# Kernel optimization log

Measured on AMD Instinct MI355X. Metric: run time of the kernel, lower is better.

## Reference

```python
import jax, jax.numpy as jnp
import numpy as np

INPUT_SIZE = 200
HIDDEN_SIZE = 100
B, T = 64, 2048


def setup_inputs() -> dict:
    key = jax.random.key(0)
    k_x, k_wi, k_wh, k_bi, k_bh = jax.random.split(key, 5)
    s = 1.0 / np.sqrt(HIDDEN_SIZE)  # PyTorch LSTM init range
    x = jax.random.normal(k_x, (B, T, INPUT_SIZE), dtype=jnp.float32)
    W_ih = jax.random.uniform(k_wi, (4 * HIDDEN_SIZE, INPUT_SIZE), minval=-s, maxval=s, dtype=jnp.float32)
    W_hh = jax.random.uniform(k_wh, (4 * HIDDEN_SIZE, HIDDEN_SIZE), minval=-s, maxval=s, dtype=jnp.float32)
    b_ih = jax.random.uniform(k_bi, (4 * HIDDEN_SIZE,), minval=-s, maxval=s, dtype=jnp.float32)
    b_hh = jax.random.uniform(k_bh, (4 * HIDDEN_SIZE,), minval=-s, maxval=s, dtype=jnp.float32)
    return {"x": x, "W_ih": W_ih, "W_hh": W_hh, "b_ih": b_ih, "b_hh": b_hh}


def reference(x, W_ih, W_hh, b_ih, b_hh):
    # Single-layer batch_first LSTM; returns output[:, -1] == final hidden state h_T.
    Bb, Tt, _ = x.shape
    H = W_hh.shape[1]
    # Precompute input projections for all timesteps: [T, B, 4H]
    xg = jnp.einsum('bti,gi->tbg', x, W_ih) + (b_ih + b_hh)

    def step(carry, xt):
        h, c = carry
        gates = xt + h @ W_hh.T  # [B, 4H]
        i, f, g, o = jnp.split(gates, 4, axis=-1)  # PyTorch gate order: i,f,g,o
        i = jax.nn.sigmoid(i)
        f = jax.nn.sigmoid(f)
        g = jnp.tanh(g)
        o = jax.nn.sigmoid(o)
        c = f * c + i * g
        h = o * jnp.tanh(c)
        return (h, c), None

    h0 = jnp.zeros((Bb, H), dtype=x.dtype)
    c0 = jnp.zeros((Bb, H), dtype=x.dtype)
    (hT, _), _ = jax.lax.scan(step, (h0, c0), xg)
    return hT  # [B, H]
```

## Files before the change

### kernel.cpp

```cpp
#include <hip/hip_runtime.h>
#include <math.h>


#define T_TOTAL 2048
#define B_SZ 64
#define IN_SZ 200
#define H_SZ 100
#define GP 512
#define KP 112
#define NPROD 192
#define NBLK 256

typedef float v2f __attribute__((ext_vector_type(2)));

__device__ __forceinline__ float sigf(float x) {
    return __builtin_amdgcn_rcpf(1.f + __expf(-x));
}

#define QSWAP(x, ctrl) \
    __int_as_float(__builtin_amdgcn_mov_dpp(__float_as_int(x), ctrl, 0xF, 0xF, true))
#define QBCAST(x, ctrl) QSWAP(x, ctrl)

#define LDS_BARRIER()                                          \
    do {                                                       \
        asm volatile("s_waitcnt lgkmcnt(0)" ::: "memory");     \
        __builtin_amdgcn_s_barrier();                          \
    } while (0)

__global__ void prep_kernel(const float* __restrict__ W_ih,
                            const float* __restrict__ W_hh,
                            const float* __restrict__ b_ih,
                            const float* __restrict__ b_hh,
                            float* __restrict__ Wt,
                            float* __restrict__ bias,
                            float* __restrict__ Whp,
                            unsigned int* __restrict__ sync) {
    int idx = blockIdx.x * 256 + threadIdx.x;
    if (idx < IN_SZ * GP) {
        int k = idx >> 9;
        int g = idx & (GP - 1);
        Wt[idx] = (g < 400) ? W_ih[g * IN_SZ + k] : 0.f;
    }
    if (idx < GP) bias[idx] = (idx < 400) ? (b_ih[idx] + b_hh[idx]) : 0.f;
    if (idx < 400 * KP) {
        int g = idx / KP;
        int k = idx - g * KP;
        Whp[idx] = (k < H_SZ) ? W_hh[g * H_SZ + k] : 0.f;
    }
    if (idx < 64) sync[idx] = 0u;
}

__global__ __attribute__((amdgpu_flat_work_group_size(512, 512), amdgpu_waves_per_eu(2, 2)))
void fused_kernel(const float* __restrict__ x,
                  const float* __restrict__ Wt,
                  const float* __restrict__ bias,
                  const float* __restrict__ Whp,
                  float* __restrict__ xg,
                  float* __restrict__ out,
                  unsigned int* __restrict__ sync,
                  int TC, int NB, int nch) {
    __shared__ __align__(16) float hlds[2][KP];
    __shared__ __align__(16) float xTc[2][50][68];
    __shared__ __align__(16) float4 LW[50][32];

    const int bid = blockIdx.x;
    const int tid = threadIdx.x;
    unsigned int* done = sync;
    unsigned int* freed = sync + 32;
    const size_t slot_sz = (size_t)B_SZ * TC * GP;

    if (bid < B_SZ) {
        const int b = bid;
        const int q = tid >> 2;
        const int s4 = tid & 3;
        const bool active = (q < H_SZ);
        const int qc = active ? q : (H_SZ - 1);
        const bool o1 = (s4 & 1) != 0;
        const bool o2 = (s4 & 2) != 0;
        const float asc  = (s4 == 2) ? 2.f : 1.f;
        const float amul = (s4 == 2) ? 2.f : 1.f;
        const float aadd = (s4 == 2) ? -1.f : 0.f;

        v2f w[4][14];
        if (active) {
            const v2f* W2 = (const v2f*)Whp;
#pragma unroll
            for (int g = 0; g < 4; ++g) {
                const v2f* row = W2 + (size_t)(g * H_SZ + q) * (KP / 2) + s4 * 14;
#pragma unroll
                for (int m = 0; m < 14; ++m) w[g][m] = row[m];
            }
        } else {
#pragma unroll
            for (int g = 0; g < 4; ++g)
#pragma unroll
                for (int m = 0; m < 14; ++m) { w[g][m].x = 0.f; w[g][m].y = 0.f; }
        }

        float c = 0.f;
        if (tid < KP) hlds[0][tid] = 0.f;
        if (tid < KP - H_SZ) hlds[1][H_SZ + tid] = 0.f;
        __syncthreads();

        const size_t lane_off = (size_t)(s4 * H_SZ + qc);
        float hval = 0.f;

#define LSTM_STEP(XB, RB, WB, KOFF)                                            \
    {                                                                          \
        const float4* hb4 = (const float4*)&hlds[RB][s4 * 28];                 \
        float4 h4 = hb4[0];                                                    \
        v2f hlo; hlo.x = h4.x; hlo.y = h4.y;                                   \
        v2f hhi; hhi.x = h4.z; hhi.y = h4.w;                                   \
        v2f a0[4], a1[4];                                                      \
        _Pragma("unroll") for (int g = 0; g < 4; ++g) {                        \
            a0[g] = hlo * w[g][0];                                             \
            a1[g] = hhi * w[g][1];                                             \
        }                                                                      \
        _Pragma("unroll") for (int m = 1; m < 7; ++m) {                        \
            h4 = hb4[m];                                                       \
            hlo.x = h4.x; hlo.y = h4.y;                                        \
            hhi.x = h4.z; hhi.y = h4.w;                                        \
            _Pragma("unroll") for (int g = 0; g < 4; ++g) {                    \
                a0[g] = __builtin_elementwise_fma(hlo, w[g][2 * m], a0[g]);    \
                a1[g] = __builtin_elementwise_fma(hhi, w[g][2 * m + 1], a1[g]);\
            }                                                                  \
        }                                                                      \
        float p[4];                                                            \
        _Pragma("unroll") for (int g = 0; g < 4; ++g) {                        \
            v2f sv = a0[g] + a1[g];                                            \
            p[g] = sv.x + sv.y;                                                \
        }                                                                      \
        float e01 = o1 ? p[0] : p[1];                                          \
        float r01 = (o1 ? p[1] : p[0]) + QSWAP(e01, 0xB1);                     \
        float e23 = o1 ? p[2] : p[3];                                          \
        float r23 = (o1 ? p[3] : p[2]) + QSWAP(e23, 0xB1);                     \
        float ecx = o2 ? r01 : r23;                                            \
        float dwn = (o2 ? r23 : r01) + QSWAP(ecx, 0x4E) + XB;                  \
        XB = xq[(KOFF) * GP];                                                  \
        float act = __builtin_fmaf(sigf(asc * dwn), amul, aadd);               \
        float vi = QBCAST(act, 0x00);                                          \
        float vf = QBCAST(act, 0x55);                                          \
        float vg = QBCAST(act, 0xAA);                                          \
        float vo = QBCAST(act, 0xFF);                                          \
        c = __builtin_fmaf(vf, c, vi * vg);                                    \
        float tcv = __builtin_fmaf(sigf(2.f * c), 2.f, -1.f);                  \
        hval = vo * tcv;                                                       \
        if (active && s4 == 0) hlds[WB][q] = hval;                             \
        LDS_BARRIER();                                                         \
    }

        for (int k = 0; k < nch; ++k) {
            if (tid == 0) {
                while (atomicAdd(&done[k], 0u) < (unsigned)NPROD)
                    __builtin_amdgcn_s_sleep(8);
                __threadfence();
            }
            __syncthreads();

            const float* xp = xg + (size_t)(k % NB) * slot_sz + (size_t)b * TC * GP + lane_off;
            float xr0 = xp[0 * GP];
            float xr1 = xp[1 * GP];
            float xr2 = xp[2 * GP];
            float xr3 = xp[3 * GP];
            const float* xq = xp + 4 * GP;

            for (int tl = 0; tl < TC; tl += 4) {
                LSTM_STEP(xr0, 0, 1, 0);
                LSTM_STEP(xr1, 1, 0, 1);
                LSTM_STEP(xr2, 0, 1, 2);
                LSTM_STEP(xr3, 1, 0, 3);
                xq += 4 * GP;
            }
            if (tid == 0) atomicAdd(&freed[k], 1u);
        }
#undef LSTM_STEP

        if (active && s4 == 0) out[b * H_SZ + q] = hval;

    } else {
        const int pid = bid - B_SZ;
        const int h = tid >> 8;
        const int t2 = tid & 255;
        const int gt = t2 & 15;
        const int tt = t2 >> 4;
        const int TPB = TC >> 7;
        const int njobs = B_SZ * TPB * 4;
        const float2* x2 = (const float2*)x;
        const float4* Wt4 = (const float4*)Wt;
        const float4* bias4 = (const float4*)bias;

        for (int k = 0; k < nch; ++k) {
            if (k >= NB) {
                if (tid == 0)
                    while (atomicAdd(&freed[k - NB], 0u) < (unsigned)B_SZ)
                        __builtin_amdgcn_s_sleep(8);
                __syncthreads();
            }
            float* slot = xg + (size_t)(k % NB) * slot_sz;
            float4* slot4 = (float4*)slot;

            for (int job = pid; job < njobs; job += NPROD) {
                const int b = job / (TPB * 4);
                const int r = job - b * (TPB * 4);
                const int tj = r >> 2;
                const int gblk = r & 3;
                const int tl0 = tj * 128 + h * 64;
                const int ta0 = k * TC + tl0;

                v2f acc[4][4];
#pragma unroll
                for (int tr = 0; tr < 4; ++tr)
#pragma unroll
                    for (int hh = 0; hh < 4; ++hh) { acc[tr][hh].x = 0.f; acc[tr][hh].y = 0.f; }

                for (int kc = 0; kc < 4; ++kc) {
                    for (int idx = t2; idx < 64 * 25; idx += 256) {
                        int row = idx / 25, c2 = idx % 25;
                        float2 v = x2[(size_t)(b * T_TOTAL + ta0 + row) * (IN_SZ / 2) + kc * 25 + c2];
                        xTc[h][c2 * 2][row] = v.x;
                        xTc[h][c2 * 2 + 1][row] = v.y;
                    }
                    for (int idx = tid; idx < 50 * 32; idx += 512) {
                        int kk = idx >> 5, cc = idx & 31;
                        LW[kk][cc] = Wt4[(size_t)(kc * 50 + kk) * (GP / 4) + gblk * 32 + cc];
                    }
                    __syncthreads();

#pragma unroll 5
                    for (int kk = 0; kk < 50; ++kk) {
                        float4 xv = *(const float4*)&xTc[h][kk][tt * 4];
                        float4 w0 = LW[kk][gt];
                        float4 w1 = LW[kk][16 + gt];
                        v2f wv[4];
                        wv[0].x = w0.x; wv[0].y = w0.y; wv[1].x = w0.z; wv[1].y = w0.w;
                        wv[2].x = w1.x; wv[2].y = w1.y; wv[3].x = w1.z; wv[3].y = w1.w;
                        float xa[4] = {xv.x, xv.y, xv.z, xv.w};
#pragma unroll
                        for (int tr = 0; tr < 4; ++tr) {
                            v2f xs; xs.x = xa[tr]; xs.y = xa[tr];
#pragma unroll
                            for (int hh = 0; hh < 4; ++hh)
                                acc[tr][hh] = __builtin_elementwise_fma(xs, wv[hh], acc[tr][hh]);
                        }
                    }
                    __syncthreads();
                }

                float4 b0 = bias4[gblk * 32 + gt];
                float4 b1 = bias4[gblk * 32 + 16 + gt];
#pragma unroll
                for (int tr = 0; tr < 4; ++tr) {
                    int trow = tl0 + tt * 4 + tr;
                    size_t o = (size_t)(b * TC + trow) * (GP / 4) + gblk * 32;
                    float4 v0 = make_float4(acc[tr][0].x + b0.x, acc[tr][0].y + b0.y,
                                            acc[tr][1].x + b0.z, acc[tr][1].y + b0.w);
                    float4 v1 = make_float4(acc[tr][2].x + b1.x, acc[tr][2].y + b1.y,
                                            acc[tr][3].x + b1.z, acc[tr][3].y + b1.w);
                    slot4[o + gt] = v0;
                    slot4[o + 16 + gt] = v1;
                }
            }
            __syncthreads();
            if (tid == 0) {
                __threadfence();
                atomicAdd(&done[k], 1u);
            }
        }
    }
}

extern "C" void kernel_launch(void* const* d_in, const int* in_sizes, int n_in,
                              void* d_out, int out_size, void* d_ws, size_t ws_size,
                              hipStream_t stream) {
    const float* x    = (const float*)d_in[0];
    const float* W_ih = (const float*)d_in[1];
    const float* W_hh = (const float*)d_in[2];
    const float* b_ih = (const float*)d_in[3];
    const float* b_hh = (const float*)d_in[4];
    float* out = (float*)d_out;

    char* ws = (char*)d_ws;
    float* Wt           = (float*)(ws);
    float* bias         = (float*)(ws + 409600);
    float* Whp          = (float*)(ws + 411648);
    unsigned int* sync  = (unsigned int*)(ws + 590848);
    float* xgbuf        = (float*)(ws + 593920);

    size_t avail = (ws_size > 593920 + 8192) ? (ws_size - 593920 - 8192) : 0;
    int TC, NB;
    if (avail >= 2ull * B_SZ * 256 * GP * 4)      { TC = 256; NB = 2; }
    else if (avail >= 2ull * B_SZ * 128 * GP * 4) { TC = 128; NB = 2; }
    else                                          { TC = 128; NB = 1; }
    int nch = T_TOTAL / TC;

    prep_kernel<<<400, 256, 0, stream>>>(W_ih, W_hh, b_ih, b_hh, Wt, bias, Whp, sync);
    fused_kernel<<<NBLK, 512, 0, stream>>>(x, Wt, bias, Whp, xgbuf, out, sync,
                                           TC, NB, nch);
}
```

Baseline: 1.263 ms.

## Halve block size: two lanes per hidden unit in LSTM recurrence

Each hidden unit's recurrent dot product is now split across 2 lanes instead of 4, so a block needs 256 threads and each lane holds twice as many W_hh weights in registers. Gate reduction drops to a single DPP swap, and the gate activations are split so each lane computes two gates. The producer blocks shrink to 256 threads and process one 64-timestep tile per job instead of two halves. The aim is to cut cross-lane shuffle work and barrier cost on the serial critical path. The trade-off is a longer per-lane FMA chain and higher register pressure, allowed by waves_per_eu 1.

```diff
diff --git a/kernel.cpp b/kernel.cpp
--- a/kernel.cpp
+++ b/kernel.cpp
@@ -19,7 +19,6 @@
 
 #define QSWAP(x, ctrl) \
     __int_as_float(__builtin_amdgcn_mov_dpp(__float_as_int(x), ctrl, 0xF, 0xF, true))
-#define QBCAST(x, ctrl) QSWAP(x, ctrl)
 
 #define LDS_BARRIER()                                          \
     do {                                                       \
@@ -50,7 +49,7 @@
     if (idx < 64) sync[idx] = 0u;
 }
 
-__global__ __attribute__((amdgpu_flat_work_group_size(512, 512), amdgpu_waves_per_eu(2, 2)))
+__global__ __attribute__((amdgpu_flat_work_group_size(256, 256), amdgpu_waves_per_eu(1, 1)))
 void fused_kernel(const float* __restrict__ x,
                   const float* __restrict__ Wt,
                   const float* __restrict__ bias,
@@ -60,7 +59,7 @@
                   unsigned int* __restrict__ sync,
                   int TC, int NB, int nch) {
     __shared__ __align__(16) float hlds[2][KP];
-    __shared__ __align__(16) float xTc[2][50][68];
+    __shared__ __align__(16) float xTc[50][68];
     __shared__ __align__(16) float4 LW[50][32];
 
     const int bid = blockIdx.x;
@@ -71,30 +70,28 @@
 
     if (bid < B_SZ) {
         const int b = bid;
-        const int q = tid >> 2;
-        const int s4 = tid & 3;
+        const int q = tid >> 1;
+        const int s2 = tid & 1;
         const bool active = (q < H_SZ);
         const int qc = active ? q : (H_SZ - 1);
-        const bool o1 = (s4 & 1) != 0;
-        const bool o2 = (s4 & 2) != 0;
-        const float asc  = (s4 == 2) ? 2.f : 1.f;
-        const float amul = (s4 == 2) ? 2.f : 1.f;
-        const float aadd = (s4 == 2) ? -1.f : 0.f;
-
-        v2f w[4][14];
+        const float bsc  = (s2 == 0) ? 2.f : 1.f;
+        const float bmul = (s2 == 0) ? 2.f : 1.f;
+        const float badd = (s2 == 0) ? -1.f : 0.f;
+
+        v2f w[4][28];
         if (active) {
             const v2f* W2 = (const v2f*)Whp;
 #pragma unroll
             for (int g = 0; g < 4; ++g) {
-                const v2f* row = W2 + (size_t)(g * H_SZ + q) * (KP / 2) + s4 * 14;
-#pragma unroll
-                for (int m = 0; m < 14; ++m) w[g][m] = row[m];
+                const v2f* row = W2 + (size_t)(g * H_SZ + q) * (KP / 2) + s2 * 28;
+#pragma unroll
+                for (int m = 0; m < 28; ++m) w[g][m] = row[m];
             }
         } else {
 #pragma unroll
             for (int g = 0; g < 4; ++g)
 #pragma unroll
-                for (int m = 0; m < 14; ++m) { w[g][m].x = 0.f; w[g][m].y = 0.f; }
+                for (int m = 0; m < 28; ++m) { w[g][m].x = 0.f; w[g][m].y = 0.f; }
         }
 
         float c = 0.f;
@@ -102,12 +99,12 @@
         if (tid < KP - H_SZ) hlds[1][H_SZ + tid] = 0.f;
         __syncthreads();
 
-        const size_t lane_off = (size_t)(s4 * H_SZ + qc);
+        const size_t lane_off = (size_t)(s2 * H_SZ + qc);
         float hval = 0.f;
 
-#define LSTM_STEP(XB, RB, WB, KOFF)                                            \
+#define LSTM_STEP(XA, XB, RB, WB, KOFF)                                        \
     {                                                                          \
-        const float4* hb4 = (const float4*)&hlds[RB][s4 * 28];                 \
+        const float4* hb4 = (const float4*)&hlds[RB][s2 * 56];                 \
         float4 h4 = hb4[0];                                                    \
         v2f hlo; hlo.x = h4.x; hlo.y = h4.y;                                   \
         v2f hhi; hhi.x = h4.z; hhi.y = h4.w;                                   \
@@ -116,7 +113,7 @@
             a0[g] = hlo * w[g][0];                                             \
             a1[g] = hhi * w[g][1];                                             \
         }                                                                      \
-        _Pragma("unroll") for (int m = 1; m < 7; ++m) {                        \
+        _Pragma("unroll") for (int m = 1; m < 14; ++m) {                       \
             h4 = hb4[m];                                                       \
             hlo.x = h4.x; hlo.y = h4.y;                                        \
             hhi.x = h4.z; hhi.y = h4.w;                                        \
@@ -130,22 +127,26 @@
             v2f sv = a0[g] + a1[g];                                            \
             p[g] = sv.x + sv.y;                                                \
         }                                                                      \
-        float e01 = o1 ? p[0] : p[1];                                          \
-        float r01 = (o1 ? p[1] : p[0]) + QSWAP(e01, 0xB1);                     \
-        float e23 = o1 ? p[2] : p[3];                                          \
-        float r23 = (o1 ? p[3] : p[2]) + QSWAP(e23, 0xB1);                     \
-        float ecx = o2 ? r01 : r23;                                            \
-        float dwn = (o2 ? r23 : r01) + QSWAP(ecx, 0x4E) + XB;                  \
-        XB = xq[(KOFF) * GP];                                                  \
-        float act = __builtin_fmaf(sigf(asc * dwn), amul, aadd);               \
-        float vi = QBCAST(act, 0x00);                                          \
-        float vf = QBCAST(act, 0x55);                                          \
-        float vg = QBCAST(act, 0xAA);                                          \
-        float vo = QBCAST(act, 0xFF);                                          \
+        float ea = s2 ? p[0] : p[1];                                           \
+        float ra = (s2 ? p[1] : p[0]) + QSWAP(ea, 0xB1);                       \
+        float eb = s2 ? p[2] : p[3];                                           \
+        float rb = (s2 ? p[3] : p[2]) + QSWAP(eb, 0xB1);                       \
+        float dwa = ra + XA;                                                   \
+        float dwb = rb + XB;                                                   \
+        XA = xq[(KOFF) * GP];                                                  \
+        XB = xq[(KOFF) * GP + 2 * H_SZ];                                       \
+        float acta = sigf(dwa);                                                \
+        float actb = __builtin_fmaf(sigf(bsc * dwb), bmul, badd);              \
+        float fa = QSWAP(acta, 0xB1);                                          \
+        float fb = QSWAP(actb, 0xB1);                                          \
+        float vi = s2 ? fa : acta;                                             \
+        float vf = s2 ? acta : fa;                                             \
+        float vg = s2 ? fb : actb;                                             \
+        float vo = s2 ? actb : fb;                                             \
         c = __builtin_fmaf(vf, c, vi * vg);                                    \
         float tcv = __builtin_fmaf(sigf(2.f * c), 2.f, -1.f);                  \
         hval = vo * tcv;                                                       \
-        if (active && s4 == 0) hlds[WB][q] = hval;                             \
+        if (active && s2 == 0) hlds[WB][q] = hval;                             \
         LDS_BARRIER();                                                         \
     }
 
@@ -158,32 +159,30 @@
             __syncthreads();
 
             const float* xp = xg + (size_t)(k % NB) * slot_sz + (size_t)b * TC * GP + lane_off;
-            float xr0 = xp[0 * GP];
-            float xr1 = xp[1 * GP];
-            float xr2 = xp[2 * GP];
-            float xr3 = xp[3 * GP];
+            float xa0 = xp[0 * GP], xb0 = xp[0 * GP + 2 * H_SZ];
+            float xa1 = xp[1 * GP], xb1 = xp[1 * GP + 2 * H_SZ];
+            float xa2 = xp[2 * GP], xb2 = xp[2 * GP + 2 * H_SZ];
+            float xa3 = xp[3 * GP], xb3 = xp[3 * GP + 2 * H_SZ];
             const float* xq = xp + 4 * GP;
 
             for (int tl = 0; tl < TC; tl += 4) {
-                LSTM_STEP(xr0, 0, 1, 0);
-                LSTM_STEP(xr1, 1, 0, 1);
-                LSTM_STEP(xr2, 0, 1, 2);
-                LSTM_STEP(xr3, 1, 0, 3);
+                LSTM_STEP(xa0, xb0, 0, 1, 0);
+                LSTM_STEP(xa1, xb1, 1, 0, 1);
+                LSTM_STEP(xa2, xb2, 0, 1, 2);
+                LSTM_STEP(xa3, xb3, 1, 0, 3);
                 xq += 4 * GP;
             }
             if (tid == 0) atomicAdd(&freed[k], 1u);
         }
 #undef LSTM_STEP
 
-        if (active && s4 == 0) out[b * H_SZ + q] = hval;
+        if (active && s2 == 0) out[b * H_SZ + q] = hval;
 
     } else {
         const int pid = bid - B_SZ;
-        const int h = tid >> 8;
-        const int t2 = tid & 255;
-        const int gt = t2 & 15;
-        const int tt = t2 >> 4;
-        const int TPB = TC >> 7;
+        const int gt = tid & 15;
+        const int tt = tid >> 4;
+        const int TPB = TC >> 6;
         const int njobs = B_SZ * TPB * 4;
         const float2* x2 = (const float2*)x;
         const float4* Wt4 = (const float4*)Wt;
@@ -204,7 +203,7 @@
                 const int r = job - b * (TPB * 4);
                 const int tj = r >> 2;
                 const int gblk = r & 3;
-                const int tl0 = tj * 128 + h * 64;
+                const int tl0 = tj * 64;
                 const int ta0 = k * TC + tl0;
 
                 v2f acc[4][4];
@@ -214,13 +213,13 @@
                     for (int hh = 0; hh < 4; ++hh) { acc[tr][hh].x = 0.f; acc[tr][hh].y = 0.f; }
 
                 for (int kc = 0; kc < 4; ++kc) {
-                    for (int idx = t2; idx < 64 * 25; idx += 256) {
+                    for (int idx = tid; idx < 64 * 25; idx += 256) {
                         int row = idx / 25, c2 = idx % 25;
                         float2 v = x2[(size_t)(b * T_TOTAL + ta0 + row) * (IN_SZ / 2) + kc * 25 + c2];
-                        xTc[h][c2 * 2][row] = v.x;
-                        xTc[h][c2 * 2 + 1][row] = v.y;
+                        xTc[c2 * 2][row] = v.x;
+                        xTc[c2 * 2 + 1][row] = v.y;
                     }
-                    for (int idx = tid; idx < 50 * 32; idx += 512) {
+                    for (int idx = tid; idx < 50 * 32; idx += 256) {
                         int kk = idx >> 5, cc = idx & 31;
                         LW[kk][cc] = Wt4[(size_t)(kc * 50 + kk) * (GP / 4) + gblk * 32 + cc];
                     }
@@ -228,7 +227,7 @@
 
 #pragma unroll 5
                     for (int kk = 0; kk < 50; ++kk) {
-                        float4 xv = *(const float4*)&xTc[h][kk][tt * 4];
+                        float4 xv = *(const float4*)&xTc[kk][tt * 4];
                         float4 w0 = LW[kk][gt];
                         float4 w1 = LW[kk][16 + gt];
                         v2f wv[4];
@@ -294,6 +293,6 @@
     int nch = T_TOTAL / TC;
 
     prep_kernel<<<400, 256, 0, stream>>>(W_ih, W_hh, b_ih, b_hh, Wt, bias, Whp, sync);
-    fused_kernel<<<NBLK, 512, 0, stream>>>(x, Wt, bias, Whp, xgbuf, out, sync,
+    fused_kernel<<<NBLK, 256, 0, stream>>>(x, Wt, bias, Whp, xgbuf, out, sync,
                                            TC, NB, nch);
 }
```

After: 1.890 ms. 1.5x slower.

## Transpose xg slot layout to gate-major so consumers load four timesteps per float4

Applied to the files above, without the earlier changes.

Producer blocks now write the precomputed input projections in a [batch][gate][time] layout instead of [batch][time][gate], storing four consecutive timesteps per float4. The recurrent consumer then loads one float4 per lane covering four steps, rather than issuing one scalar strided global load per step. The goal is fewer load instructions and less latency on the serial recurrence critical path. The cost is that producer stores become strided across gates, which may make the writes less coalesced.

```diff
diff --git a/kernel.cpp b/kernel.cpp
--- a/kernel.cpp
+++ b/kernel.cpp
@@ -102,10 +102,10 @@
         if (tid < KP - H_SZ) hlds[1][H_SZ + tid] = 0.f;
         __syncthreads();
 
-        const size_t lane_off = (size_t)(s4 * H_SZ + qc);
+        const int gate = s4 * H_SZ + qc;
         float hval = 0.f;
 
-#define LSTM_STEP(XB, RB, WB, KOFF)                                            \
+#define LSTM_STEP(XV, RB, WB)                                                  \
     {                                                                          \
         const float4* hb4 = (const float4*)&hlds[RB][s4 * 28];                 \
         float4 h4 = hb4[0];                                                    \
@@ -135,8 +135,7 @@
         float e23 = o1 ? p[2] : p[3];                                          \
         float r23 = (o1 ? p[3] : p[2]) + QSWAP(e23, 0xB1);                     \
         float ecx = o2 ? r01 : r23;                                            \
-        float dwn = (o2 ? r23 : r01) + QSWAP(ecx, 0x4E) + XB;                  \
-        XB = xq[(KOFF) * GP];                                                  \
+        float dwn = (o2 ? r23 : r01) + QSWAP(ecx, 0x4E) + (XV);                \
         float act = __builtin_fmaf(sigf(asc * dwn), amul, aadd);               \
         float vi = QBCAST(act, 0x00);                                          \
         float vf = QBCAST(act, 0x55);                                          \
@@ -157,19 +156,28 @@
             }
             __syncthreads();
 
-            const float* xp = xg + (size_t)(k % NB) * slot_sz + (size_t)b * TC * GP + lane_off;
-            float xr0 = xp[0 * GP];
-            float xr1 = xp[1 * GP];
-            float xr2 = xp[2 * GP];
-            float xr3 = xp[3 * GP];
-            const float* xq = xp + 4 * GP;
-
-            for (int tl = 0; tl < TC; tl += 4) {
-                LSTM_STEP(xr0, 0, 1, 0);
-                LSTM_STEP(xr1, 1, 0, 1);
-                LSTM_STEP(xr2, 0, 1, 2);
-                LSTM_STEP(xr3, 1, 0, 3);
-                xq += 4 * GP;
+            const float4* xr = (const float4*)(xg + (size_t)(k % NB) * slot_sz
+                                               + ((size_t)b * GP + gate) * TC);
+            float4 X0 = xr[0];
+            float4 X1 = xr[1];
+            float4 X2 = xr[2];
+            float4 X3 = xr[3];
+            const float4* xq4 = xr + 4;
+
+            for (int tl = 0; tl < TC; tl += 16) {
+                LSTM_STEP(X0.x, 0, 1); LSTM_STEP(X0.y, 1, 0);
+                LSTM_STEP(X0.z, 0, 1); LSTM_STEP(X0.w, 1, 0);
+                X0 = xq4[0];
+                LSTM_STEP(X1.x, 0, 1); LSTM_STEP(X1.y, 1, 0);
+                LSTM_STEP(X1.z, 0, 1); LSTM_STEP(X1.w, 1, 0);
+                X1 = xq4[1];
+                LSTM_STEP(X2.x, 0, 1); LSTM_STEP(X2.y, 1, 0);
+                LSTM_STEP(X2.z, 0, 1); LSTM_STEP(X2.w, 1, 0);
+                X2 = xq4[2];
+                LSTM_STEP(X3.x, 0, 1); LSTM_STEP(X3.y, 1, 0);
+                LSTM_STEP(X3.z, 0, 1); LSTM_STEP(X3.w, 1, 0);
+                X3 = xq4[3];
+                xq4 += 4;
             }
             if (tid == 0) atomicAdd(&freed[k], 1u);
         }
@@ -197,7 +205,6 @@
                 __syncthreads();
             }
             float* slot = xg + (size_t)(k % NB) * slot_sz;
-            float4* slot4 = (float4*)slot;
 
             for (int job = pid; job < njobs; job += NPROD) {
                 const int b = job / (TPB * 4);
@@ -246,18 +253,25 @@
                     __syncthreads();
                 }
 
+                const int t0l = tl0 + tt * 4;
                 float4 b0 = bias4[gblk * 32 + gt];
                 float4 b1 = bias4[gblk * 32 + 16 + gt];
-#pragma unroll
-                for (int tr = 0; tr < 4; ++tr) {
-                    int trow = tl0 + tt * 4 + tr;
-                    size_t o = (size_t)(b * TC + trow) * (GP / 4) + gblk * 32;
-                    float4 v0 = make_float4(acc[tr][0].x + b0.x, acc[tr][0].y + b0.y,
-                                            acc[tr][1].x + b0.z, acc[tr][1].y + b0.w);
-                    float4 v1 = make_float4(acc[tr][2].x + b1.x, acc[tr][2].y + b1.y,
-                                            acc[tr][3].x + b1.z, acc[tr][3].y + b1.w);
-                    slot4[o + gt] = v0;
-                    slot4[o + 16 + gt] = v1;
+                float bb0[4] = {b0.x, b0.y, b0.z, b0.w};
+                float bb1[4] = {b1.x, b1.y, b1.z, b1.w};
+                const size_t base0 = ((size_t)b * GP + (size_t)((gblk * 32 + gt) * 4)) * TC + t0l;
+                const size_t base1 = ((size_t)b * GP + (size_t)((gblk * 32 + 16 + gt) * 4)) * TC + t0l;
+#pragma unroll
+                for (int j = 0; j < 4; ++j) {
+                    float4 v0 = make_float4(acc[0][j >> 1][j & 1] + bb0[j],
+                                            acc[1][j >> 1][j & 1] + bb0[j],
+                                            acc[2][j >> 1][j & 1] + bb0[j],
+                                            acc[3][j >> 1][j & 1] + bb0[j]);
+                    float4 v1 = make_float4(acc[0][2 + (j >> 1)][j & 1] + bb1[j],
+                                            acc[1][2 + (j >> 1)][j & 1] + bb1[j],
+                                            acc[2][2 + (j >> 1)][j & 1] + bb1[j],
+                                            acc[3][2 + (j >> 1)][j & 1] + bb1[j]);
+                    *(float4*)(slot + base0 + (size_t)j * TC) = v0;
+                    *(float4*)(slot + base1 + (size_t)j * TC) = v1;
                 }
             }
             __syncthreads();
```

After: 1.242 ms. No clear change (-1.7%).
